# Kernel tuning notes

Hardware: AMD Instinct MI355X
Metric: run time of the kernel (lower is better)

Reference implementation:

```python
import jax, jax.numpy as jnp
import numpy as np

B, N, K, H, NHEADS, NIN = 4, 2000, 30, 128, 4, 256
DFF = 4 * H
EPS = 1e-6


def layer_norm(x, gain, bias):
    # torch .var() defaults to unbiased (ddof=1); denominator is (sigma + eps)
    mu = x.mean(-1, keepdims=True)
    sigma = jnp.sqrt(x.var(-1, ddof=1, keepdims=True) + EPS)
    return gain * (x - mu) / (sigma + EPS) + bias


def setup_inputs() -> dict:
    key = jax.random.key(0)
    ks = jax.random.split(key, 10)
    s = 0.05
    h_v = jax.random.normal(ks[0], (B, N, H), jnp.float32)
    h_e = jax.random.normal(ks[1], (B, N, K, NIN), jnp.float32)
    mask_attend = (jax.random.uniform(ks[2], (B, N, K)) < 0.9).astype(jnp.float32)
    mask_attend = mask_attend.at[..., 0].set(1.0)  # avoid all-masked rows -> NaN softmax
    mask_v = (jax.random.uniform(ks[3], (B, N)) < 0.95).astype(jnp.float32)
    return {
        "h_v": h_v,
        "h_e": h_e,
        "mask_v": mask_v,
        "mask_attend": mask_attend,
        "W_Q": jax.random.normal(ks[4], (H, H), jnp.float32) * s,
        "W_K": jax.random.normal(ks[5], (H, NIN), jnp.float32) * s,
        "W_V": jax.random.normal(ks[6], (H, NIN), jnp.float32) * s,
        "W_O": jax.random.normal(ks[7], (H, H), jnp.float32) * s,
        "gain0": jnp.ones((H,), jnp.float32),
        "bias0": jnp.zeros((H,), jnp.float32),
        "gain1": jnp.ones((H,), jnp.float32),
        "bias1": jnp.zeros((H,), jnp.float32),
        "W_in": jax.random.normal(ks[8], (DFF, H), jnp.float32) * s,
        "b_in": jnp.zeros((DFF,), jnp.float32),
        "W_out": jax.random.normal(ks[9], (H, DFF), jnp.float32) * s,
        "b_out": jnp.zeros((H,), jnp.float32),
    }


def reference(h_v, h_e, mask_v, mask_attend, W_Q, W_K, W_V, W_O,
              gain0, bias0, gain1, bias1, W_in, b_in, W_out, b_out):
    d = H // NHEADS
    # Neighbor attention (dropout is identity at inference)
    Q = (h_v @ W_Q.T).reshape(B, N, NHEADS, d)          # [B,N,h,d]
    Kp = (h_e @ W_K.T).reshape(B, N, K, NHEADS, d)      # [B,N,K,h,d]
    Vp = (h_e @ W_V.T).reshape(B, N, K, NHEADS, d)      # [B,N,K,h,d]
    logits = jnp.einsum('bnhd,bnkhd->bnhk', Q, Kp) / np.sqrt(d)
    mask = mask_attend[:, :, None, :]                   # [B,N,1,K] broadcast over heads
    neg_inf = jnp.finfo(logits.dtype).min
    attend = jax.nn.softmax(jnp.where(mask > 0, logits, neg_inf), axis=-1) * mask
    h_upd = jnp.einsum('bnhk,bnkhd->bnhd', attend, Vp).reshape(B, N, H)
    dh = h_upd @ W_O.T
    h = layer_norm(h_v + dh, gain0, bias0)
    # Position-wise FFN
    dh = jax.nn.relu(h @ W_in.T + b_in) @ W_out.T + b_out
    h = layer_norm(h + dh, gain1, bias1)
    return mask_v[..., None] * h
```

## Files before the change

### kernel.cpp

```cpp
#include <hip/hip_runtime.h>
#include <math.h>

#define TK 30
#define TH 128
#define TNIN 256
#define TDFF 512
#define NTOK 8000
#define ROWP 264

typedef __attribute__((ext_vector_type(8))) short short8v;
typedef __attribute__((ext_vector_type(4))) short short4v;
typedef __attribute__((ext_vector_type(4))) float f32x4;

constexpr float LN_EPS = 1e-6f;
constexpr float NEG_INF = -3.402823466e38f;
constexpr float INV_SQRT_D = 0.17677669529663687f;

static __device__ __forceinline__ unsigned short f2bf(float f) {
  unsigned u = __float_as_uint(f);
  u = u + 0x7fffu + ((u >> 16) & 1u);
  return (unsigned short)(u >> 16);
}
static __device__ __forceinline__ float bf2f(unsigned short s) {
  return __uint_as_float(((unsigned)s) << 16);
}
static __device__ __forceinline__ void gload16(const void* gsrc, void* ldst) {
  __builtin_amdgcn_global_load_lds(
      (const __attribute__((address_space(1))) unsigned int*)gsrc,
      (__attribute__((address_space(3))) unsigned int*)ldst, 16, 0, 0);
}

__global__ void conv_weights_kernel(const float* __restrict__ W_K,
                                    const float* __restrict__ W_V,
                                    const float* __restrict__ W_Q,
                                    const float* __restrict__ W_O,
                                    const float* __restrict__ W_in,
                                    const float* __restrict__ W_out,
                                    unsigned short* __restrict__ Wc2,
                                    unsigned short* __restrict__ Wq2,
                                    unsigned short* __restrict__ Wp2,
                                    unsigned short* __restrict__ Wi2,
                                    unsigned short* __restrict__ Wo2)
{
  int idx = blockIdx.x * 256 + threadIdx.x;
  if (idx < 65536) {
    int e = idx >> 3, j = idx & 7;
    int kk = e >> 10, n = (e >> 6) & 15, lane = e & 63;
    int r = n*16 + (lane & 15);
    int c = kk*32 + (lane >> 4)*8 + j;
    float v = (r < TH) ? W_K[(size_t)r*TNIN + c] : W_V[(size_t)(r-TH)*TNIN + c];
    Wc2[idx] = f2bf(v);
  } else if (idx < 81920) {
    int i2 = idx - 65536;
    int e = i2 >> 3, j = i2 & 7;
    int kk = e >> 9, n = (e >> 6) & 7, lane = e & 63;
    int r = n*16 + (lane & 15);
    int c = kk*32 + (lane >> 4)*8 + j;
    Wq2[i2] = f2bf(W_Q[(size_t)r*TH + c]);
  } else if (idx < 98304) {
    int ip = idx - 81920;
    int e = ip >> 3, j = ip & 7;
    int kk = e >> 9, n = (e >> 6) & 7, lane = e & 63;
    int r = n*16 + (lane & 15);
    int c = kk*32 + (lane >> 4)*8 + j;
    Wp2[ip] = f2bf(W_O[(size_t)r*TH + c]);
  } else if (idx < 163840) {
    int i3 = idx - 98304;
    int e = i3 >> 3, j = i3 & 7;
    int ks = e >> 11, n = (e >> 6) & 31, lane = e & 63;
    int r = n*16 + (lane & 15);
    int c = ks*32 + (lane >> 4)*8 + j;
    Wi2[i3] = f2bf(W_in[(size_t)r*TH + c]);
  } else {
    int i4 = idx - 163840;
    int e = i4 >> 3, j = i4 & 7;
    int ks = e >> 9, n = (e >> 6) & 7, lane = e & 63;
    int r = n*16 + (lane & 15);
    int c = ks*32 + (lane >> 4)*8 + j;
    Wo2[i4] = f2bf(W_out[(size_t)r*TDFF + c]);
  }
}

__global__ __launch_bounds__(512, 4) void kvattn_kernel(
    const float* __restrict__ A, const unsigned short* __restrict__ Wc2,
    const unsigned short* __restrict__ Wq2, const float* __restrict__ h_v,
    const float* __restrict__ mask_attend, float* __restrict__ ul)
{
  const int tid  = threadIdx.x;
  const int wave = tid >> 6;
  const int lane = tid & 63;
  const int lm   = lane & 15;
  const int lgp  = lane >> 4;
  const int mh   = wave >> 2;
  const int nq   = wave & 3;
  const int bn0  = blockIdx.x * 4;

  __shared__ __align__(16) char smem[73728];
  unsigned short* Bl  = (unsigned short*)smem;
  unsigned short* Al  = (unsigned short*)(smem + 49152);
  unsigned short* KVs = (unsigned short*)smem;
  float* att = (float*)(smem + 67584);
  float* hvp = (float*)(smem + 69632);
  float* qvp = (float*)(smem + 71680);

  if (tid < 128) {
    int tok = tid >> 5, q = tid & 31;
    *(float4*)&hvp[tok*128 + q*4] = *(const float4*)&h_v[(size_t)(bn0 + tok)*TH + q*4];
  }

  const int rowa = tid >> 2, cga = tid & 3;
  const int rowc = (rowa > 119) ? 119 : rowa;
  const float* aptr = A + ((size_t)blockIdx.x*120 + rowc)*TNIN + cga*8;

  #define ISSUE_B(K)                                                             \
    { gload16(Wc2 + (size_t)(K)*8192 + tid*8,       &Bl[((K)%3)*8192 + tid*8]);  \
      gload16(Wc2 + (size_t)(K)*8192 + (tid+512)*8, &Bl[((K)%3)*8192 + (tid+512)*8]); }

  #define WRITE_A(K, S)                                                     \
    { short8v w;                                                            \
      w[0]=(short)f2bf(ra[S][0].x); w[1]=(short)f2bf(ra[S][0].y);           \
      w[2]=(short)f2bf(ra[S][0].z); w[3]=(short)f2bf(ra[S][0].w);           \
      w[4]=(short)f2bf(ra[S][1].x); w[5]=(short)f2bf(ra[S][1].y);           \
      w[6]=(short)f2bf(ra[S][1].z); w[7]=(short)f2bf(ra[S][1].w);           \
      *(short8v*)&Al[(((K)&1)*128 + rowa)*40 + cga*8] = w; }

  float4 ra[3][2];
  f32x4 acc[4][4] = {};

  ra[0][0] = *(const float4*)(aptr + 0);
  ra[0][1] = *(const float4*)(aptr + 4);
  ISSUE_B(0);
  ISSUE_B(1);
  ra[1][0] = *(const float4*)(aptr + 32);
  ra[1][1] = *(const float4*)(aptr + 36);
  ra[2][0] = *(const float4*)(aptr + 64);
  ra[2][1] = *(const float4*)(aptr + 68);
  WRITE_A(0, 0);

  #pragma unroll
  for (int k = 0; k < 8; ++k) {
    if (k == 7)      asm volatile("s_waitcnt vmcnt(0)" ::: "memory");
    else if (k == 6) asm volatile("s_waitcnt vmcnt(4)" ::: "memory");
    else             asm volatile("s_waitcnt vmcnt(6)" ::: "memory");
    __builtin_amdgcn_s_barrier();

    if (k < 6) ISSUE_B(k+2);
    if (k < 5) {
      ra[k%3][0] = *(const float4*)(aptr + (k+3)*32);
      ra[k%3][1] = *(const float4*)(aptr + (k+3)*32 + 4);
    }

    short8v af[4];
    #pragma unroll
    for (int m = 0; m < 4; ++m)
      af[m] = *(const short8v*)&Al[((k&1)*128 + mh*64 + m*16 + lm)*40 + lgp*8];

    #pragma unroll
    for (int n = 0; n < 4; ++n) {
      short8v b = *(const short8v*)&Bl[(k%3)*8192 + ((nq*4 + n)*64 + lane)*8];
      #pragma unroll
      for (int m = 0; m < 4; ++m)
        acc[m][n] = __builtin_amdgcn_mfma_f32_16x16x32_bf16(b, af[m], acc[m][n], 0, 0, 0);
    }

    if (k < 7) WRITE_A(k+1, (k+1)%3);
  }
  #undef ISSUE_B
  #undef WRITE_A

  __syncthreads();

  #pragma unroll
  for (int m = 0; m < 4; ++m) {
    int row = mh*64 + m*16 + lm;
    #pragma unroll
    for (int n = 0; n < 4; ++n) {
      int col = nq*64 + n*16 + lgp*4;
      short4v p;
      p[0]=(short)f2bf(acc[m][n][0]); p[1]=(short)f2bf(acc[m][n][1]);
      p[2]=(short)f2bf(acc[m][n][2]); p[3]=(short)f2bf(acc[m][n][3]);
      *(short4v*)&KVs[row*ROWP + col] = p;
    }
  }

  {
    f32x4 qacc = {};
    const int tokc = (lm < 4) ? lm : 3;
    #pragma unroll
    for (int ks = 0; ks < 4; ++ks) {
      short8v wq = *(const short8v*)(Wq2 + ((size_t)(ks*8 + wave)*64 + lane)*8);
      const float* hp = hvp + tokc*128 + ks*32 + lgp*8;
      float4 lo = *(const float4*)hp;
      float4 hi = *(const float4*)(hp + 4);
      short8v ha;
      ha[0]=(short)f2bf(lo.x); ha[1]=(short)f2bf(lo.y);
      ha[2]=(short)f2bf(lo.z); ha[3]=(short)f2bf(lo.w);
      ha[4]=(short)f2bf(hi.x); ha[5]=(short)f2bf(hi.y);
      ha[6]=(short)f2bf(hi.z); ha[7]=(short)f2bf(hi.w);
      qacc = __builtin_amdgcn_mfma_f32_16x16x32_bf16(wq, ha, qacc, 0, 0, 0);
    }
    if (lm < 4) *(f32x4*)&qvp[lm*128 + wave*16 + lgp*4] = qacc;
  }
  __syncthreads();

  {
    int tok = tid >> 7, h = (tid >> 5) & 3, k = tid & 31;
    int gtok = bn0 + tok;
    float s = 0.f;
    float ma = 0.f;
    if (k < TK) {
      const float* qp = &qvp[tok*128 + h*32];
      const unsigned short* kp = &KVs[(tok*TK + k)*ROWP + h*32];
      #pragma unroll
      for (int j = 0; j < 4; ++j) {
        short8v kf = *(const short8v*)(kp + j*8);
        float4 qa = *(const float4*)(qp + j*8);
        float4 qb = *(const float4*)(qp + j*8 + 4);
        s += qa.x*bf2f((unsigned short)kf[0]) + qa.y*bf2f((unsigned short)kf[1])
           + qa.z*bf2f((unsigned short)kf[2]) + qa.w*bf2f((unsigned short)kf[3])
           + qb.x*bf2f((unsigned short)kf[4]) + qb.y*bf2f((unsigned short)kf[5])
           + qb.z*bf2f((unsigned short)kf[6]) + qb.w*bf2f((unsigned short)kf[7]);
      }
      ma = mask_attend[(size_t)gtok*TK + k];
    }
    bool ok = (k < TK) && (ma > 0.f);
    float val = ok ? s * INV_SQRT_D : NEG_INF;
    float mm = val;
    #pragma unroll
    for (int d = 16; d >= 1; d >>= 1) mm = fmaxf(mm, __shfl_xor(mm, d, 32));
    float e = ok ? expf(val - mm) : 0.f;
    float ss = e;
    #pragma unroll
    for (int d = 16; d >= 1; d >>= 1) ss += __shfl_xor(ss, d, 32);
    att[(tok*4 + h)*32 + k] = e / ss;
  }
  __syncthreads();

  {
    int tok = tid >> 7, c = tid & 127;
    int gtok = bn0 + tok;
    const float* ar = &att[(tok*4 + (c >> 5))*32];
    const unsigned short* vb = &KVs[tok*TK*ROWP + TH + c];
    float u = 0.f;
    #pragma unroll
    for (int k = 0; k < TK; ++k)
      u += ar[k] * bf2f(vb[k*ROWP]);
    ul[(size_t)gtok*TH + c] = u;
  }
}

__global__ __launch_bounds__(256) void ffn_all_kernel(
    const float* __restrict__ ul, const unsigned short* __restrict__ Wp2,
    const float* __restrict__ h_v,
    const float* __restrict__ gain0, const float* __restrict__ bias0,
    const unsigned short* __restrict__ Wi2, const unsigned short* __restrict__ Wo2,
    const float* __restrict__ b_in, const float* __restrict__ b_out,
    const float* __restrict__ gain1, const float* __restrict__ bias1,
    const float* __restrict__ mask_v, float* __restrict__ out)
{
  const int tid  = threadIdx.x;
  const int tok0 = blockIdx.x * 32;
  const int wave = tid >> 6;
  const int lane = tid & 63;
  const int lm   = lane & 15;
  const int lgp  = lane >> 4;

  __shared__ __align__(16) char smem[78336];
  unsigned short* Bst = (unsigned short*)smem;
  unsigned short* At  = (unsigned short*)(smem + 32768);
  unsigned short* Zs  = (unsigned short*)(smem + 41472);
  float* bin  = (float*)(smem + 74752);
  float* part = (float*)(smem + 76800);
  float* red  = (float*)(smem + 77824);

  for (int t = tid; t < 1024; t += 256) {
    int row = t >> 5, q = t & 31;
    float4 v = *(const float4*)&ul[(size_t)(tok0+row)*TH + q*4];
    short4v w;
    w[0]=(short)f2bf(v.x); w[1]=(short)f2bf(v.y);
    w[2]=(short)f2bf(v.z); w[3]=(short)f2bf(v.w);
    *(short4v*)&At[row*136 + q*4] = w;
  }
  if (tid < 128) *(float4*)&bin[tid*4] = *(const float4*)&b_in[tid*4];
  #pragma unroll
  for (int p = 0; p < 8; ++p)
    gload16(Wp2 + (size_t)(tid + p*256)*8, &Bst[(tid + p*256)*8]);
  asm volatile("s_waitcnt vmcnt(0)" ::: "memory");
  __syncthreads();

  f32x4 acco[2][2] = {};
  #pragma unroll
  for (int ks = 0; ks < 4; ++ks) {
    short8v a0 = *(const short8v*)&At[lm*136      + ks*32 + lgp*8];
    short8v a1 = *(const short8v*)&At[(16+lm)*136 + ks*32 + lgp*8];
    #pragma unroll
    for (int n = 0; n < 2; ++n) {
      short8v b = *(const short8v*)&Bst[((size_t)(ks*8 + wave*2 + n)*64 + lane)*8];
      acco[0][n] = __builtin_amdgcn_mfma_f32_16x16x32_bf16(b, a0, acco[0][n], 0, 0, 0);
      acco[1][n] = __builtin_amdgcn_mfma_f32_16x16x32_bf16(b, a1, acco[1][n], 0, 0, 0);
    }
  }

  f32x4 hn[2][2];
  {
    f32x4 x[2][2];
    float s1r[2] = {0.f, 0.f}, s2r[2] = {0.f, 0.f};
    #pragma unroll
    for (int m = 0; m < 2; ++m) {
      int row = m*16 + lm;
      #pragma unroll
      for (int n = 0; n < 2; ++n) {
        int col = (wave*2 + n)*16 + lgp*4;
        float4 hv = *(const float4*)&h_v[(size_t)(tok0+row)*TH + col];
        x[m][n][0] = acco[m][n][0] + hv.x;
        x[m][n][1] = acco[m][n][1] + hv.y;
        x[m][n][2] = acco[m][n][2] + hv.z;
        x[m][n][3] = acco[m][n][3] + hv.w;
        #pragma unroll
        for (int r = 0; r < 4; ++r) {
          s1r[m] += x[m][n][r];
          s2r[m] += x[m][n][r]*x[m][n][r];
        }
      }
    }
    #pragma unroll
    for (int m = 0; m < 2; ++m) {
      s1r[m] += __shfl_xor(s1r[m], 16); s2r[m] += __shfl_xor(s2r[m], 16);
      s1r[m] += __shfl_xor(s1r[m], 32); s2r[m] += __shfl_xor(s2r[m], 32);
    }
    if (lgp == 0) {
      part[(lm*4      + wave)*2 + 0] = s1r[0];
      part[(lm*4      + wave)*2 + 1] = s2r[0];
      part[((16+lm)*4 + wave)*2 + 0] = s1r[1];
      part[((16+lm)*4 + wave)*2 + 1] = s2r[1];
    }
    __syncthreads();
    if (tid < 32) {
      float s1 = 0.f, s2 = 0.f;
      #pragma unroll
      for (int w = 0; w < 4; ++w) { s1 += part[(tid*4+w)*2]; s2 += part[(tid*4+w)*2+1]; }
      float mu  = s1*(1.f/128.f);
      float var = (s2 - 128.f*mu*mu)*(1.f/127.f);
      red[tid*2]   = mu;
      red[tid*2+1] = 1.f/(sqrtf(var+LN_EPS)+LN_EPS);
    }
    __syncthreads();
    #pragma unroll
    for (int m = 0; m < 2; ++m) {
      int row = m*16 + lm;
      float mu = red[row*2], inv = red[row*2+1];
      #pragma unroll
      for (int n = 0; n < 2; ++n) {
        int col = (wave*2 + n)*16 + lgp*4;
        float4 g = *(const float4*)&gain0[col];
        float4 b = *(const float4*)&bias0[col];
        hn[m][n][0] = g.x*(x[m][n][0]-mu)*inv + b.x;
        hn[m][n][1] = g.y*(x[m][n][1]-mu)*inv + b.y;
        hn[m][n][2] = g.z*(x[m][n][2]-mu)*inv + b.z;
        hn[m][n][3] = g.w*(x[m][n][3]-mu)*inv + b.w;
        short4v p;
        p[0]=(short)f2bf(hn[m][n][0]); p[1]=(short)f2bf(hn[m][n][1]);
        p[2]=(short)f2bf(hn[m][n][2]); p[3]=(short)f2bf(hn[m][n][3]);
        *(short4v*)&At[row*136 + col] = p;
      }
    }
  }
  __syncthreads();

  f32x4 acc1[2][8] = {};
  #pragma unroll
  for (int ks = 0; ks < 4; ++ks) {
    #pragma unroll
    for (int p = 0; p < 8; ++p)
      gload16(Wi2 + (size_t)ks*16384 + (tid + p*256)*8, &Bst[(tid + p*256)*8]);
    asm volatile("s_waitcnt vmcnt(0)" ::: "memory");
    __syncthreads();

    short8v a0 = *(const short8v*)&At[lm*136      + ks*32 + lgp*8];
    short8v a1 = *(const short8v*)&At[(16+lm)*136 + ks*32 + lgp*8];
    #pragma unroll
    for (int n = 0; n < 8; ++n) {
      short8v b = *(const short8v*)&Bst[((wave*8 + n)*64 + lane)*8];
      acc1[0][n] = __builtin_amdgcn_mfma_f32_16x16x32_bf16(b, a0, acc1[0][n], 0, 0, 0);
      acc1[1][n] = __builtin_amdgcn_mfma_f32_16x16x32_bf16(b, a1, acc1[1][n], 0, 0, 0);
    }
    __syncthreads();
  }

  #pragma unroll
  for (int m = 0; m < 2; ++m) {
    int row = m*16 + lm;
    #pragma unroll
    for (int n = 0; n < 8; ++n) {
      int col = (wave*8 + n)*16 + lgp*4;
      float4 bv = *(const float4*)&bin[col];
      short4v p;
      p[0]=(short)f2bf(fmaxf(acc1[m][n][0] + bv.x, 0.f));
      p[1]=(short)f2bf(fmaxf(acc1[m][n][1] + bv.y, 0.f));
      p[2]=(short)f2bf(fmaxf(acc1[m][n][2] + bv.z, 0.f));
      p[3]=(short)f2bf(fmaxf(acc1[m][n][3] + bv.w, 0.f));
      *(short4v*)&Zs[row*520 + col] = p;
    }
  }
  __syncthreads();

  f32x4 acc2[2][2] = {};
  #pragma unroll
  for (int ks2 = 0; ks2 < 8; ++ks2) {
    #pragma unroll
    for (int p = 0; p < 4; ++p)
      gload16(Wo2 + (size_t)ks2*8192 + (tid + p*256)*8, &Bst[(tid + p*256)*8]);
    asm volatile("s_waitcnt vmcnt(0)" ::: "memory");
    __syncthreads();

    #pragma unroll
    for (int s = 0; s < 2; ++s) {
      int ks = ks2*2 + s;
      short8v a0 = *(const short8v*)&Zs[lm*520      + ks*32 + lgp*8];
      short8v a1 = *(const short8v*)&Zs[(16+lm)*520 + ks*32 + lgp*8];
      #pragma unroll
      for (int n = 0; n < 2; ++n) {
        short8v b = *(const short8v*)&Bst[(s*4096) + ((wave*2 + n)*64 + lane)*8];
        acc2[0][n] = __builtin_amdgcn_mfma_f32_16x16x32_bf16(b, a0, acc2[0][n], 0, 0, 0);
        acc2[1][n] = __builtin_amdgcn_mfma_f32_16x16x32_bf16(b, a1, acc2[1][n], 0, 0, 0);
      }
    }
    __syncthreads();
  }

  {
    f32x4 x[2][2];
    float s1r[2] = {0.f, 0.f}, s2r[2] = {0.f, 0.f};
    #pragma unroll
    for (int m = 0; m < 2; ++m) {
      #pragma unroll
      for (int n = 0; n < 2; ++n) {
        int col = (wave*2 + n)*16 + lgp*4;
        float4 bo = *(const float4*)&b_out[col];
        x[m][n][0] = acc2[m][n][0] + bo.x + hn[m][n][0];
        x[m][n][1] = acc2[m][n][1] + bo.y + hn[m][n][1];
        x[m][n][2] = acc2[m][n][2] + bo.z + hn[m][n][2];
        x[m][n][3] = acc2[m][n][3] + bo.w + hn[m][n][3];
        #pragma unroll
        for (int r = 0; r < 4; ++r) {
          s1r[m] += x[m][n][r];
          s2r[m] += x[m][n][r]*x[m][n][r];
        }
      }
    }
    #pragma unroll
    for (int m = 0; m < 2; ++m) {
      s1r[m] += __shfl_xor(s1r[m], 16); s2r[m] += __shfl_xor(s2r[m], 16);
      s1r[m] += __shfl_xor(s1r[m], 32); s2r[m] += __shfl_xor(s2r[m], 32);
    }
    if (lgp == 0) {
      part[(lm*4      + wave)*2 + 0] = s1r[0];
      part[(lm*4      + wave)*2 + 1] = s2r[0];
      part[((16+lm)*4 + wave)*2 + 0] = s1r[1];
      part[((16+lm)*4 + wave)*2 + 1] = s2r[1];
    }
    __syncthreads();
    if (tid < 32) {
      float s1 = 0.f, s2 = 0.f;
      #pragma unroll
      for (int w = 0; w < 4; ++w) { s1 += part[(tid*4+w)*2]; s2 += part[(tid*4+w)*2+1]; }
      float mu  = s1*(1.f/128.f);
      float var = (s2 - 128.f*mu*mu)*(1.f/127.f);
      red[tid*2]   = mu;
      red[tid*2+1] = 1.f/(sqrtf(var+LN_EPS)+LN_EPS);
    }
    __syncthreads();
    #pragma unroll
    for (int m = 0; m < 2; ++m) {
      int row = m*16 + lm;
      float mu = red[row*2], inv = red[row*2+1];
      float mv = mask_v[tok0 + row];
      #pragma unroll
      for (int n = 0; n < 2; ++n) {
        int col = (wave*2 + n)*16 + lgp*4;
        float4 g = *(const float4*)&gain1[col];
        float4 b = *(const float4*)&bias1[col];
        float4 y;
        y.x = mv*(g.x*(x[m][n][0]-mu)*inv + b.x);
        y.y = mv*(g.y*(x[m][n][1]-mu)*inv + b.y);
        y.z = mv*(g.z*(x[m][n][2]-mu)*inv + b.z);
        y.w = mv*(g.w*(x[m][n][3]-mu)*inv + b.w);
        *(float4*)&out[(size_t)(tok0+row)*TH + col] = y;
      }
    }
  }
}

extern "C" void kernel_launch(void* const* d_in, const int* in_sizes, int n_in,
                              void* d_out, int out_size, void* d_ws, size_t ws_size,
                              hipStream_t stream)
{
  const float* h_v         = (const float*)d_in[0];
  const float* h_e         = (const float*)d_in[1];
  const float* mask_v      = (const float*)d_in[2];
  const float* mask_attend = (const float*)d_in[3];
  const float* W_Q   = (const float*)d_in[4];
  const float* W_K   = (const float*)d_in[5];
  const float* W_V   = (const float*)d_in[6];
  const float* W_O   = (const float*)d_in[7];
  const float* gain0 = (const float*)d_in[8];
  const float* bias0 = (const float*)d_in[9];
  const float* gain1 = (const float*)d_in[10];
  const float* bias1 = (const float*)d_in[11];
  const float* W_in  = (const float*)d_in[12];
  const float* b_in  = (const float*)d_in[13];
  const float* W_out = (const float*)d_in[14];
  const float* b_out = (const float*)d_in[15];

  float* out = (float*)d_out;
  char* ws = (char*)d_ws;
  unsigned short* Wc2 = (unsigned short*)ws;
  unsigned short* Wq2 = (unsigned short*)(ws + 131072);
  unsigned short* Wp2 = (unsigned short*)(ws + 163840);
  unsigned short* Wi2 = (unsigned short*)(ws + 196608);
  unsigned short* Wo2 = (unsigned short*)(ws + 327680);
  float* ul = (float*)(ws + 458752);

  conv_weights_kernel<<<896, 256, 0, stream>>>(W_K, W_V, W_Q, W_O, W_in, W_out,
                                               Wc2, Wq2, Wp2, Wi2, Wo2);
  kvattn_kernel<<<NTOK/4, 512, 0, stream>>>(h_e, Wc2, Wq2, h_v, mask_attend, ul);
  ffn_all_kernel<<<NTOK/32, 256, 0, stream>>>(ul, Wp2, h_v, gain0, bias0,
                                              Wi2, Wo2, b_in, b_out,
                                              gain1, bias1, mask_v, out);
}
```

Before: 80.92 us.

## Double-buffer FFN weight streaming and raise MFMA wave priority in KV kernel

The FFN kernel now prefetches the next W_in/W_out chunk into a second LDS buffer while MFMAs run on the current one. It also issues the first W_in load alongside W_proj, and keeps a single barrier per step instead of two. Separately, s_setprio brackets the MFMA loop in the KV projection kernel. The aim is to hide global weight-load latency behind compute. The cost is LDS use growing from about 78KB to about 143KB, which lowers occupancy to one block per CU, and the reduced synchronisation risks subtle race conditions.

```diff
diff --git a/kernel.cpp b/kernel.cpp
--- a/kernel.cpp
+++ b/kernel.cpp
@@ -155,6 +155,7 @@
     for (int m = 0; m < 4; ++m)
       af[m] = *(const short8v*)&Al[((k&1)*128 + mh*64 + m*16 + lm)*40 + lgp*8];
 
+    __builtin_amdgcn_s_setprio(1);
     #pragma unroll
     for (int n = 0; n < 4; ++n) {
       short8v b = *(const short8v*)&Bl[(k%3)*8192 + ((nq*4 + n)*64 + lane)*8];
@@ -162,6 +163,7 @@
       for (int m = 0; m < 4; ++m)
         acc[m][n] = __builtin_amdgcn_mfma_f32_16x16x32_bf16(b, af[m], acc[m][n], 0, 0, 0);
     }
+    __builtin_amdgcn_s_setprio(0);
 
     if (k < 7) WRITE_A(k+1, (k+1)%3);
   }
@@ -265,13 +267,14 @@
   const int lm   = lane & 15;
   const int lgp  = lane >> 4;
 
-  __shared__ __align__(16) char smem[78336];
-  unsigned short* Bst = (unsigned short*)smem;
-  unsigned short* At  = (unsigned short*)(smem + 32768);
-  unsigned short* Zs  = (unsigned short*)(smem + 41472);
-  float* bin  = (float*)(smem + 74752);
-  float* part = (float*)(smem + 76800);
-  float* red  = (float*)(smem + 77824);
+  __shared__ __align__(16) char smem[143616];
+  unsigned short* Wp  = (unsigned short*)smem;
+  unsigned short* Wst = (unsigned short*)(smem + 32768);
+  unsigned short* At  = (unsigned short*)(smem + 98304);
+  unsigned short* Zs  = (unsigned short*)(smem + 107008);
+  float* bin  = (float*)(smem + 140288);
+  float* part = (float*)(smem + 142336);
+  float* red  = (float*)(smem + 143360);
 
   for (int t = tid; t < 1024; t += 256) {
     int row = t >> 5, q = t & 31;
@@ -284,8 +287,12 @@
   if (tid < 128) *(float4*)&bin[tid*4] = *(const float4*)&b_in[tid*4];
   #pragma unroll
   for (int p = 0; p < 8; ++p)
-    gload16(Wp2 + (size_t)(tid + p*256)*8, &Bst[(tid + p*256)*8]);
-  asm volatile("s_waitcnt vmcnt(0)" ::: "memory");
+    gload16(Wp2 + (size_t)(tid + p*256)*8, &Wp[(tid + p*256)*8]);
+  #pragma unroll
+  for (int p = 0; p < 8; ++p)
+    gload16(Wi2 + (size_t)(tid + p*256)*8, &Wst[(tid + p*256)*8]);
+
+  asm volatile("s_waitcnt vmcnt(8)" ::: "memory");
   __syncthreads();
 
   f32x4 acco[2][2] = {};
@@ -295,7 +302,7 @@
     short8v a1 = *(const short8v*)&At[(16+lm)*136 + ks*32 + lgp*8];
     #pragma unroll
     for (int n = 0; n < 2; ++n) {
-      short8v b = *(const short8v*)&Bst[((size_t)(ks*8 + wave*2 + n)*64 + lane)*8];
+      short8v b = *(const short8v*)&Wp[((size_t)(ks*8 + wave*2 + n)*64 + lane)*8];
       acco[0][n] = __builtin_amdgcn_mfma_f32_16x16x32_bf16(b, a0, acco[0][n], 0, 0, 0);
       acco[1][n] = __builtin_amdgcn_mfma_f32_16x16x32_bf16(b, a1, acco[1][n], 0, 0, 0);
     }
@@ -365,26 +372,31 @@
       }
     }
   }
-  __syncthreads();
 
   f32x4 acc1[2][8] = {};
   #pragma unroll
   for (int ks = 0; ks < 4; ++ks) {
-    #pragma unroll
-    for (int p = 0; p < 8; ++p)
-      gload16(Wi2 + (size_t)ks*16384 + (tid + p*256)*8, &Bst[(tid + p*256)*8]);
     asm volatile("s_waitcnt vmcnt(0)" ::: "memory");
-    __syncthreads();
+    __builtin_amdgcn_s_barrier();
+    if (ks < 3) {
+      #pragma unroll
+      for (int p = 0; p < 8; ++p)
+        gload16(Wi2 + (size_t)(ks+1)*16384 + (tid + p*256)*8,
+                &Wst[((ks+1)&1)*16384 + (tid + p*256)*8]);
+    } else {
+      #pragma unroll
+      for (int p = 0; p < 4; ++p)
+        gload16(Wo2 + (size_t)(tid + p*256)*8, &Wst[(tid + p*256)*8]);
+    }
 
     short8v a0 = *(const short8v*)&At[lm*136      + ks*32 + lgp*8];
     short8v a1 = *(const short8v*)&At[(16+lm)*136 + ks*32 + lgp*8];
     #pragma unroll
     for (int n = 0; n < 8; ++n) {
-      short8v b = *(const short8v*)&Bst[((wave*8 + n)*64 + lane)*8];
+      short8v b = *(const short8v*)&Wst[(ks&1)*16384 + ((wave*8 + n)*64 + lane)*8];
       acc1[0][n] = __builtin_amdgcn_mfma_f32_16x16x32_bf16(b, a0, acc1[0][n], 0, 0, 0);
       acc1[1][n] = __builtin_amdgcn_mfma_f32_16x16x32_bf16(b, a1, acc1[1][n], 0, 0, 0);
     }
-    __syncthreads();
   }
 
   #pragma unroll
@@ -402,16 +414,18 @@
       *(short4v*)&Zs[row*520 + col] = p;
     }
   }
-  __syncthreads();
 
   f32x4 acc2[2][2] = {};
   #pragma unroll
   for (int ks2 = 0; ks2 < 8; ++ks2) {
-    #pragma unroll
-    for (int p = 0; p < 4; ++p)
-      gload16(Wo2 + (size_t)ks2*8192 + (tid + p*256)*8, &Bst[(tid + p*256)*8]);
     asm volatile("s_waitcnt vmcnt(0)" ::: "memory");
-    __syncthreads();
+    __builtin_amdgcn_s_barrier();
+    if (ks2 < 7) {
+      #pragma unroll
+      for (int p = 0; p < 4; ++p)
+        gload16(Wo2 + (size_t)(ks2+1)*8192 + (tid + p*256)*8,
+                &Wst[((ks2+1)&1)*8192 + (tid + p*256)*8]);
+    }
 
     #pragma unroll
     for (int s = 0; s < 2; ++s) {
@@ -420,12 +434,11 @@
       short8v a1 = *(const short8v*)&Zs[(16+lm)*520 + ks*32 + lgp*8];
       #pragma unroll
       for (int n = 0; n < 2; ++n) {
-        short8v b = *(const short8v*)&Bst[(s*4096) + ((wave*2 + n)*64 + lane)*8];
+        short8v b = *(const short8v*)&Wst[(ks2&1)*8192 + s*4096 + ((wave*2 + n)*64 + lane)*8];
         acc2[0][n] = __builtin_amdgcn_mfma_f32_16x16x32_bf16(b, a0, acc2[0][n], 0, 0, 0);
         acc2[1][n] = __builtin_amdgcn_mfma_f32_16x16x32_bf16(b, a1, acc2[1][n], 0, 0, 0);
       }
     }
-    __syncthreads();
   }
 
   {
```

After: 79.89 us (median of 2 runs). No clear change (-1.3%).
